# Kernel optimization log

Hardware: AMD Instinct MI355X
Metric: run time of the kernel (lower is better)

The kernel has to match this reference:

```python
import jax, jax.numpy as jnp
import numpy as np

B, N, N0, HH, WW = 4, 3136, 12544, 112, 112
C_IN, C_HID, C_OUT = 128, 512, 128
EPS = 1e-6
BN_EPS = 1e-5


def _grid_idx(loc_orig, H, W):
    # loc_orig [B,N0,2] in [-1,1] -> flat grid index [B,N0]
    loc = jnp.clip(loc_orig, -1.0, 1.0) * 0.5 + 0.5
    gx = jnp.clip(jnp.round(loc[..., 0] * (W - 1)).astype(jnp.int32), 0, W - 1)
    gy = jnp.clip(jnp.round(loc[..., 1] * (H - 1)).astype(jnp.int32), 0, H - 1)
    return gy * W + gx


def token2map(tokens, loc_orig, idx_agg, H, W):
    # tokens [B,N,C] -> dense map [B,C,H,W] (count-averaged scatter)
    Bs, Nt, C = tokens.shape
    Np = loc_orig.shape[1]
    idx_hw = _grid_idx(loc_orig, H, W)                       # [B,N0]
    feat = jnp.take_along_axis(tokens, idx_agg[..., None].astype(jnp.int32), axis=1)  # [B,N0,C]
    seg = (idx_hw + jnp.arange(Bs, dtype=jnp.int32)[:, None] * (H * W)).reshape(-1)
    sums = jax.ops.segment_sum(feat.reshape(Bs * Np, C), seg, num_segments=Bs * H * W)
    cnt = jax.ops.segment_sum(jnp.ones((Bs * Np,), tokens.dtype), seg, num_segments=Bs * H * W)
    out = sums / (cnt[:, None] + EPS)
    return out.reshape(Bs, H, W, C).transpose(0, 3, 1, 2)


def map2token(x_map, Nt, loc_orig, idx_agg, agg_weight, H, W):
    # x_map [B,C,H,W] -> tokens [B,N,C] (agg_weight-normalized gather+scatter)
    Bs, C = x_map.shape[0], x_map.shape[1]
    Np = loc_orig.shape[1]
    idx_hw = _grid_idx(loc_orig, H, W)                       # [B,N0]
    flat = x_map.reshape(Bs, C, H * W).transpose(0, 2, 1)    # [B,HW,C]
    feat = jnp.take_along_axis(flat, idx_hw[..., None], axis=1)  # [B,N0,C]
    seg = (idx_agg.astype(jnp.int32) + jnp.arange(Bs, dtype=jnp.int32)[:, None] * Nt).reshape(-1)
    num = jax.ops.segment_sum((agg_weight[..., None] * feat).reshape(Bs * Np, C), seg, num_segments=Bs * Nt)
    den = jax.ops.segment_sum(agg_weight.reshape(-1), seg, num_segments=Bs * Nt)
    return (num / (den[:, None] + EPS)).reshape(Bs, Nt, C)


def bn(x, g, b):
    # BatchNorm (training-mode batch stats) over x [B,C,N]
    mu = jnp.mean(x, axis=(0, 2), keepdims=True)
    var = jnp.var(x, axis=(0, 2), keepdims=True)
    return (x - mu) * jax.lax.rsqrt(var + BN_EPS) * g[None, :, None] + b[None, :, None]


def setup_inputs():
    key = jax.random.key(0)
    ks = jax.random.split(key, 8)
    x = jax.random.normal(ks[0], (B, N, C_IN), jnp.float32)
    loc_orig = jax.random.uniform(ks[1], (B, N0, 2), jnp.float32) * 2.0 - 1.0
    idx_agg = jax.random.randint(ks[2], (B, N0), 0, N, dtype=jnp.int32)
    agg_weight = jax.random.uniform(ks[3], (B, N0), jnp.float32)
    fc1_w = jax.random.normal(ks[4], (C_HID, C_IN), jnp.float32) * 0.02
    fc1_b = jnp.zeros((C_HID,), jnp.float32)
    g1 = jnp.ones((C_HID,), jnp.float32); b1 = jnp.zeros((C_HID,), jnp.float32)
    dw_w = jax.random.normal(ks[5], (C_HID, 1, 3, 3), jnp.float32) * 0.1
    dw_b = jnp.zeros((C_HID,), jnp.float32)
    dws_w = jax.random.normal(ks[6], (C_HID,), jnp.float32) * 0.1
    g2 = jnp.ones((C_HID,), jnp.float32); b2 = jnp.zeros((C_HID,), jnp.float32)
    fc2_w = jax.random.normal(ks[7], (C_OUT, C_HID), jnp.float32) * 0.02
    fc2_b = jnp.zeros((C_OUT,), jnp.float32)
    g3 = jnp.ones((C_OUT,), jnp.float32); b3 = jnp.zeros((C_OUT,), jnp.float32)
    return dict(x=x, loc_orig=loc_orig, idx_agg=idx_agg, agg_weight=agg_weight,
                fc1_w=fc1_w, fc1_b=fc1_b, g1=g1, b1=b1, dw_w=dw_w, dw_b=dw_b,
                dws_w=dws_w, g2=g2, b2=b2, fc2_w=fc2_w, fc2_b=fc2_b,
                g3=g3, b3=b3, H=HH, W=WW)


def reference(x, loc_orig, idx_agg, agg_weight, fc1_w, fc1_b, g1, b1, dw_w, dw_b,
              dws_w, g2, b2, fc2_w, fc2_b, g3, b3, H, W):
    Bs, Nt, _ = x.shape
    # fc1 (1x1 conv) -> BN -> GELU, channel-major layout [B,C,N]
    h = jnp.einsum('bnc,hc->bhn', x, fc1_w) + fc1_b[None, :, None]
    h = jax.nn.gelu(bn(h, g1, b1), approximate=False)
    # token -> map -> depthwise 3x3 -> map -> token
    x_map = token2map(h.transpose(0, 2, 1), loc_orig, idx_agg, H, W)  # [B,hid,H,W]
    x_map = jax.lax.conv_general_dilated(
        x_map, dw_w, (1, 1), 'SAME', feature_group_count=dw_w.shape[0],
        dimension_numbers=('NCHW', 'OIHW', 'NCHW')) + dw_b[None, :, None, None]
    tok = map2token(x_map, Nt, loc_orig, idx_agg, agg_weight, H, W)   # [B,N,hid]
    # depthwise 1x1 skip (per-channel scale, no bias) + map branch
    h = h * dws_w[None, :, None] + tok.transpose(0, 2, 1)
    h = jax.nn.gelu(bn(h, g2, b2), approximate=False)
    # fc2 -> BN -> GELU (dropout p=0 is identity)
    h = jnp.einsum('bhn,oh->bon', h, fc2_w) + fc2_b[None, :, None]
    h = jax.nn.gelu(bn(h, g3, b3), approximate=False)
    return h.transpose(0, 2, 1)  # [B,N,out]
```

## Files before the change

### kernel.cpp

```cpp
#include <hip/hip_runtime.h>
#include <math.h>

constexpr int kB    = 4;
constexpr int kN    = 3136;
constexpr int kN0   = 12544;
constexpr int kH    = 112, kW = 112;
constexpr int kHW   = kH * kW;
constexpr int kCIN  = 128;
constexpr int kCHID = 512;
constexpr int kCOUT = 128;
constexpr int kROWS = kB * kN;
constexpr int kPTS  = kB * kN0;
constexpr int kBHW  = kB * kHW;
constexpr int kSEG  = kBHW + kROWS;
constexpr int kScanBlks = (kSEG + 255) / 256;
constexpr int kDwBlks   = kB * kHW / 16;
constexpr float kEPS  = 1e-6f;
constexpr float kBEPS = 1e-5f;

typedef __attribute__((ext_vector_type(8))) short short8;
typedef __attribute__((ext_vector_type(4))) float f32x4;

__device__ __forceinline__ float gelu_f(float x) {
    return 0.5f * x * (1.0f + erff(x * 0.70710678118654752440f));
}
__device__ __forceinline__ float bf2f(short s) {
    union { unsigned u; float f; } v; v.u = ((unsigned)(unsigned short)s) << 16; return v.f;
}
__device__ __forceinline__ short f2bf(float f) {
    union { float f; unsigned u; } v; v.f = f;
    const unsigned r = v.u + 0x7fffu + ((v.u >> 16) & 1u);
    return (short)(r >> 16);
}

__device__ __forceinline__ void bn_coef_lds(
    const float* __restrict__ gsum, const float* __restrict__ gsq,
    const float* __restrict__ g, const float* __restrict__ bb,
    float invn, float* ssc, float* ssh)
{
    const int c = threadIdx.x * 2;
#pragma unroll
    for (int u = 0; u < 2; ++u) {
        const float m = gsum[c + u] * invn;
        const float v = fmaxf(gsq[c + u] * invn - m * m, 0.f);
        const float sc = g[c + u] * rsqrtf(v + kBEPS);
        ssc[c + u] = sc;
        ssh[c + u] = bb[c + u] - m * sc;
    }
}

template <int OUT16, int STATS>
__global__ __launch_bounds__(256) void gemm_bf16_k(
    const short* __restrict__ A, const short* __restrict__ W,
    const float* __restrict__ bias, void* __restrict__ Cv,
    float* __restrict__ gsum, float* __restrict__ gsq,
    int M, int N, int K)
{
    __shared__ float ls[64], lq[64];
    if (STATS) {
        if (threadIdx.x < 64) { ls[threadIdx.x] = 0.f; lq[threadIdx.x] = 0.f; }
        __syncthreads();
    }
    const int wave = threadIdx.x >> 6;
    const int lane = threadIdx.x & 63;
    const int r = lane & 15, kg = lane >> 4;
    const int bm = blockIdx.x * 64 + wave * 16;
    const int bn = blockIdx.y * 64;
    const short* arow = A + (size_t)(bm + r) * K + kg * 8;
    f32x4 acc[4];
#pragma unroll
    for (int j = 0; j < 4; ++j) {
        const float bz = bias[bn + j * 16 + r];
        acc[j][0] = bz; acc[j][1] = bz; acc[j][2] = bz; acc[j][3] = bz;
    }
    for (int k0 = 0; k0 < K; k0 += 32) {
        const short8 av = *(const short8*)(arow + k0);
#pragma unroll
        for (int j = 0; j < 4; ++j) {
            const short8 bv = *(const short8*)(W + (size_t)(bn + j * 16 + r) * K + k0 + kg * 8);
            acc[j] = __builtin_amdgcn_mfma_f32_16x16x32_bf16(av, bv, acc[j], 0, 0, 0);
        }
    }
#pragma unroll
    for (int j = 0; j < 4; ++j)
#pragma unroll
        for (int q = 0; q < 4; ++q) {
            const size_t idx = (size_t)(bm + kg * 4 + q) * N + bn + j * 16 + r;
            if constexpr (OUT16) ((short*)Cv)[idx] = f2bf(acc[j][q]);
            else                 ((float*)Cv)[idx] = acc[j][q];
        }
    if (STATS) {
#pragma unroll
        for (int j = 0; j < 4; ++j) {
            const float s = acc[j][0] + acc[j][1] + acc[j][2] + acc[j][3];
            const float q = acc[j][0]*acc[j][0] + acc[j][1]*acc[j][1]
                          + acc[j][2]*acc[j][2] + acc[j][3]*acc[j][3];
            atomicAdd(&ls[j * 16 + r], s);
            atomicAdd(&lq[j * 16 + r], q);
        }
        __syncthreads();
        if (threadIdx.x < 64) {
            atomicAdd(&gsum[bn + threadIdx.x], ls[threadIdx.x]);
            atomicAdd(&gsq[bn + threadIdx.x],  lq[threadIdx.x]);
        }
    }
}

__device__ __forceinline__ void cvt8(const float* __restrict__ in, short* __restrict__ out) {
    const float4 v0 = ((const float4*)in)[0];
    const float4 v1 = ((const float4*)in)[1];
    short8 o;
    o[0] = f2bf(v0.x); o[1] = f2bf(v0.y); o[2] = f2bf(v0.z); o[3] = f2bf(v0.w);
    o[4] = f2bf(v1.x); o[5] = f2bf(v1.y); o[6] = f2bf(v1.z); o[7] = f2bf(v1.w);
    *(short8*)out = o;
}

constexpr int kCVT8    = (kROWS * kCIN + 512 * 128 + 128 * 512) / 8;
constexpr int kCvtBlks = (kCVT8 + 9 * 512 + 255) / 256;
constexpr int kCntBlks = kPTS / 256;

__global__ void prep_k(const float* __restrict__ x, short* __restrict__ xb,
                       const float* __restrict__ w1, short* __restrict__ w1b,
                       const float* __restrict__ w2, short* __restrict__ w2b,
                       const float* __restrict__ dww, short* __restrict__ wTb,
                       const float* __restrict__ loc, const int* __restrict__ iagg,
                       int* __restrict__ ihw, int* __restrict__ cnt)
{
    const int blk = blockIdx.x;
    if (blk < kCvtBlks) {
        const int i = blk * 256 + threadIdx.x;
        constexpr int na = kROWS * kCIN, nb = 512 * 128;
        if (i < kCVT8) {
            int t = i * 8;
            if (t < na) { cvt8(x + t, xb + t); return; }
            t -= na;
            if (t < nb) { cvt8(w1 + t, w1b + t); return; }
            t -= nb;
            cvt8(w2 + t, w2b + t);
            return;
        }
        const int j = i - kCVT8;
        if (j < 9 * 512) {
            const int tap = j / 512, ch = j % 512;
            wTb[j] = f2bf(dww[ch * 9 + tap]);
        }
        return;
    }
    const int p = (blk - kCvtBlks) * 256 + threadIdx.x;
    if (p >= kPTS) return;
    float lx = loc[(size_t)p * 2 + 0];
    float ly = loc[(size_t)p * 2 + 1];
    lx = fminf(fmaxf(lx, -1.f), 1.f) * 0.5f + 0.5f;
    ly = fminf(fmaxf(ly, -1.f), 1.f) * 0.5f + 0.5f;
    int gx = (int)rintf(lx * (float)(kW - 1)); gx = min(max(gx, 0), kW - 1);
    int gy = (int)rintf(ly * (float)(kH - 1)); gy = min(max(gy, 0), kH - 1);
    const int idx = gy * kW + gx;
    ihw[p] = idx;
    const int b = p / kN0;
    atomicAdd(cnt + b * kHW + idx, 1);
    atomicAdd(cnt + kBHW + b * kN + iagg[p], 1);
}

__global__ __launch_bounds__(256) void scan1_k(const int* __restrict__ cnt,
                                               int* __restrict__ off, int* __restrict__ bsum)
{
    __shared__ int sh[256];
    const int t = threadIdx.x;
    const int i = blockIdx.x * 256 + t;
    const int v = (i < kSEG) ? cnt[i] : 0;
    sh[t] = v; __syncthreads();
#pragma unroll
    for (int o = 1; o < 256; o <<= 1) {
        const int tmp = (t >= o) ? sh[t - o] : 0;
        __syncthreads();
        sh[t] += tmp;
        __syncthreads();
    }
    if (i < kSEG) off[i] = sh[t] - v;
    if (t == 255) bsum[blockIdx.x] = sh[255];
}

__global__ __launch_bounds__(256) void scan23_k(int* __restrict__ off,
                                                const int* __restrict__ bsum)
{
    __shared__ int sh[256];
    const int t = threadIdx.x;
    const int v = (t < kScanBlks) ? bsum[t] : 0;
    sh[t] = v; __syncthreads();
#pragma unroll
    for (int o = 1; o < 256; o <<= 1) {
        const int tmp = (t >= o) ? sh[t - o] : 0;
        __syncthreads();
        sh[t] += tmp;
        __syncthreads();
    }
    const int add = sh[blockIdx.x] - bsum[blockIdx.x];
    const int i = blockIdx.x * 256 + t;
    if (i < kSEG) off[i] += add;
}

__global__ void fill_k(const int* __restrict__ iagg, const int* __restrict__ ihw,
                       const float* __restrict__ aw, int* __restrict__ off,
                       int* __restrict__ slotA, float* __restrict__ w_all)
{
    const int p = blockIdx.x * 256 + threadIdx.x;
    if (p >= kPTS) return;
    const int b = p / kN0;
    const int tokrow = b * kN + iagg[p];
    const int cell   = b * kHW + ihw[p];
    const int cpos = atomicAdd(off + cell, 1);
    slotA[cpos] = tokrow;
    const int tpos = atomicAdd(off + kBHW + tokrow, 1);
    slotA[tpos] = cell;
    w_all[tpos] = aw[p];
}

__global__ __launch_bounds__(256) void colstats_b(
    const short* __restrict__ X, float* __restrict__ gsum, float* __restrict__ gsq,
    int rows_per_blk)
{
    __shared__ float shs[4][512];
    __shared__ float shq[4][512];
    const int g = threadIdx.x & 63;
    const int rr = threadIdx.x >> 6;
    const int r0 = blockIdx.x * rows_per_blk;
    float s[8] = {}, q[8] = {};
    for (int r = rr; r < rows_per_blk; r += 4) {
        const short8 v = *(const short8*)(X + (size_t)(r0 + r) * kCHID + g * 8);
#pragma unroll
        for (int j = 0; j < 8; ++j) { const float f = bf2f(v[j]); s[j] += f; q[j] += f * f; }
    }
#pragma unroll
    for (int j = 0; j < 8; ++j) { shs[rr][g * 8 + j] = s[j]; shq[rr][g * 8 + j] = q[j]; }
    __syncthreads();
    const int c = threadIdx.x * 2;
    const float s0 = shs[0][c] + shs[1][c] + shs[2][c] + shs[3][c];
    const float s1 = shs[0][c+1] + shs[1][c+1] + shs[2][c+1] + shs[3][c+1];
    const float q0 = shq[0][c] + shq[1][c] + shq[2][c] + shq[3][c];
    const float q1 = shq[0][c+1] + shq[1][c+1] + shq[2][c+1] + shq[3][c+1];
    atomicAdd(&gsum[c], s0);   atomicAdd(&gsum[c+1], s1);
    atomicAdd(&gsq[c],  q0);   atomicAdd(&gsq[c+1],  q1);
}

__global__ __launch_bounds__(256) void bn_act_b(
    const short* __restrict__ in, short* __restrict__ out,
    const float* __restrict__ gsum, const float* __restrict__ gsq,
    const float* __restrict__ g, const float* __restrict__ bb, float invn)
{
    __shared__ float ssc[512], ssh[512];
    bn_coef_lds(gsum, gsq, g, bb, invn, ssc, ssh);
    __syncthreads();
    const size_t i = (size_t)blockIdx.x * 256 + threadIdx.x;
    const int c0 = (int)(i & 63) * 8;
    const short8 v = *(const short8*)(in + i * 8);
    short8 o;
#pragma unroll
    for (int j = 0; j < 8; ++j)
        o[j] = f2bf(gelu_f(fmaf(bf2f(v[j]), ssc[c0 + j], ssh[c0 + j])));
    *(short8*)(out + i * 8) = o;
}

__global__ __launch_bounds__(256) void bn_act_f128(
    const float* __restrict__ in, float* __restrict__ out,
    const float* __restrict__ gsum, const float* __restrict__ gsq,
    const float* __restrict__ g, const float* __restrict__ bb, float invn)
{
    __shared__ float ssc[128], ssh[128];
    if (threadIdx.x < 128) {
        const int c = threadIdx.x;
        const float m = gsum[c] * invn;
        const float v = fmaxf(gsq[c] * invn - m * m, 0.f);
        const float sc = g[c] * rsqrtf(v + kBEPS);
        ssc[c] = sc;
        ssh[c] = bb[c] - m * sc;
    }
    __syncthreads();
    const size_t i = (size_t)blockIdx.x * 256 + threadIdx.x;
    const int c0 = (int)(i & 31) * 4;
    float4 v = ((const float4*)in)[i];
    v.x = gelu_f(fmaf(v.x, ssc[c0 + 0], ssh[c0 + 0]));
    v.y = gelu_f(fmaf(v.y, ssc[c0 + 1], ssh[c0 + 1]));
    v.z = gelu_f(fmaf(v.z, ssc[c0 + 2], ssh[c0 + 2]));
    v.w = gelu_f(fmaf(v.w, ssc[c0 + 3], ssh[c0 + 3]));
    ((float4*)out)[i] = v;
}

__global__ __launch_bounds__(256) void gather_map_b(
    const short* __restrict__ hb, const int* __restrict__ off,
    const int* __restrict__ toklist, short* __restrict__ smap)
{
    const int lane = threadIdx.x & 63;
    const int cell = blockIdx.x * 4 + (threadIdx.x >> 6);
    const int s = cell ? off[cell - 1] : 0;
    const int e = off[cell];
    const int c0 = lane * 8;
    float a[8] = {};
    int j = s;
    for (; j + 1 < e; j += 2) {
        const int t0 = toklist[j], t1 = toklist[j + 1];
        const short8 v0 = *(const short8*)(hb + (size_t)t0 * kCHID + c0);
        const short8 v1 = *(const short8*)(hb + (size_t)t1 * kCHID + c0);
#pragma unroll
        for (int t = 0; t < 8; ++t) a[t] += bf2f(v0[t]) + bf2f(v1[t]);
    }
    if (j < e) {
        const short8 v = *(const short8*)(hb + (size_t)toklist[j] * kCHID + c0);
#pragma unroll
        for (int t = 0; t < 8; ++t) a[t] += bf2f(v[t]);
    }
    const float sc = 1.f / ((float)(e - s) + kEPS);
    short8 o;
#pragma unroll
    for (int t = 0; t < 8; ++t) o[t] = f2bf(a[t] * sc);
    *(short8*)(smap + (size_t)cell * kCHID + c0) = o;
}

__global__ __launch_bounds__(256) void dwconv_b(
    const short* __restrict__ smap, const int* __restrict__ cnt,
    const short* __restrict__ wTb, const float* __restrict__ bdw,
    short* __restrict__ convo)
{
    constexpr int kTX = kW / 2;
    constexpr int kChunk = kDwBlks / 8;
    const int wg = (blockIdx.x & 7) * kChunk + (blockIdx.x >> 3);
    const int c8 = threadIdx.x & 63;
    const int w  = wg * 4 + (threadIdx.x >> 6);
    const int b   = w / (kTX * kTX);
    const int rem = w % (kTX * kTX);
    const int ty = rem / kTX, tx = rem % kTX;
    const int y0 = ty * 2, x0 = tx * 2;
    const int gbase = b * kHW;
    const int c0 = c8 * 8;

    const int cell00 = gbase + y0 * kW + x0;
    const int2 nA = *(const int2*)(cnt + cell00);
    const int2 nB = *(const int2*)(cnt + cell00 + kW);
    const int n00 = nA.x, n01 = nA.y, n10 = nB.x, n11 = nB.y;
    if ((n00 | n01 | n10 | n11) == 0) return;

    float wf[9][8];
#pragma unroll
    for (int t = 0; t < 9; ++t) {
        const short8 wv = *(const short8*)(wTb + t * kCHID + c0);
#pragma unroll
        for (int j = 0; j < 8; ++j) wf[t][j] = bf2f(wv[j]);
    }
    float bz[8];
    {
        const float4 b0 = *(const float4*)(bdw + c0);
        const float4 b1 = *(const float4*)(bdw + c0 + 4);
        bz[0] = b0.x; bz[1] = b0.y; bz[2] = b0.z; bz[3] = b0.w;
        bz[4] = b1.x; bz[5] = b1.y; bz[6] = b1.z; bz[7] = b1.w;
    }
    float acc[2][2][8];
#pragma unroll
    for (int cy = 0; cy < 2; ++cy)
#pragma unroll
        for (int cx = 0; cx < 2; ++cx)
#pragma unroll
            for (int j = 0; j < 8; ++j) acc[cy][cx][j] = bz[j];

#pragma unroll
    for (int dy = 0; dy < 4; ++dy) {
        const int yy = y0 - 1 + dy;
        if ((unsigned)yy >= (unsigned)kH) continue;
#pragma unroll
        for (int dx = 0; dx < 4; ++dx) {
            const int xx = x0 - 1 + dx;
            if ((unsigned)xx >= (unsigned)kW) continue;
            const short8 tv = *(const short8*)(smap + (size_t)(gbase + yy * kW + xx) * kCHID + c0);
            float tf[8];
#pragma unroll
            for (int j = 0; j < 8; ++j) tf[j] = bf2f(tv[j]);
#pragma unroll
            for (int cy = 0; cy < 2; ++cy) {
                const int wy = dy - cy;
                if ((unsigned)wy >= 3u) continue;
#pragma unroll
                for (int cx = 0; cx < 2; ++cx) {
                    const int wx = dx - cx;
                    if ((unsigned)wx >= 3u) continue;
                    const float* wq = wf[wy * 3 + wx];
#pragma unroll
                    for (int j = 0; j < 8; ++j)
                        acc[cy][cx][j] = fmaf(wq[j], tf[j], acc[cy][cx][j]);
                }
            }
        }
    }
#pragma unroll
    for (int cy = 0; cy < 2; ++cy)
#pragma unroll
        for (int cx = 0; cx < 2; ++cx) {
            const int n = (cy == 0) ? (cx == 0 ? n00 : n01) : (cx == 0 ? n10 : n11);
            if (!n) continue;
            short8 o;
#pragma unroll
            for (int j = 0; j < 8; ++j) o[j] = f2bf(acc[cy][cx][j]);
            *(short8*)(convo + (size_t)(cell00 + cy * kW + cx) * kCHID + c0) = o;
        }
}

__global__ __launch_bounds__(256) void gather_tok_b(
    const short* __restrict__ convo, const int* __restrict__ off,
    const int* __restrict__ celllist, const float* __restrict__ wlist,
    const short* __restrict__ hb, const float* __restrict__ dws,
    short* __restrict__ h2)
{
    const int lane = threadIdx.x & 63;
    const int wave = threadIdx.x >> 6;
    const int t = blockIdx.x * 4 + wave;
    const int seg = kBHW + t;
    const int sbeg = off[seg - 1], send = off[seg];
    const int c0 = lane * 8;
    const float4 d0 = *(const float4*)(dws + c0);
    const float4 d1 = *(const float4*)(dws + c0 + 4);
    const float dd[8] = {d0.x, d0.y, d0.z, d0.w, d1.x, d1.y, d1.z, d1.w};
    float a[8] = {};
    float den = 0.f;
    int j = sbeg;
    for (; j + 1 < send; j += 2) {
        const float w0 = wlist[j], w1 = wlist[j + 1];
        const int   cA = celllist[j], cB = celllist[j + 1];
        den += w0 + w1;
        const short8 v0 = *(const short8*)(convo + (size_t)cA * kCHID + c0);
        const short8 v1 = *(const short8*)(convo + (size_t)cB * kCHID + c0);
#pragma unroll
        for (int k = 0; k < 8; ++k)
            a[k] += w0 * bf2f(v0[k]) + w1 * bf2f(v1[k]);
    }
    if (j < send) {
        const float w = wlist[j];
        den += w;
        const short8 v = *(const short8*)(convo + (size_t)celllist[j] * kCHID + c0);
#pragma unroll
        for (int k = 0; k < 8; ++k) a[k] = fmaf(w, bf2f(v[k]), a[k]);
    }
    const float r = 1.f / (den + kEPS);
    const short8 hv = *(const short8*)(hb + (size_t)t * kCHID + c0);
    short8 o;
#pragma unroll
    for (int k = 0; k < 8; ++k)
        o[k] = f2bf(fmaf(bf2f(hv[k]), dd[k], a[k] * r));
    *(short8*)(h2 + (size_t)t * kCHID + c0) = o;
}

extern "C" void kernel_launch(void* const* d_in, const int* in_sizes, int n_in,
                              void* d_out, int out_size, void* d_ws, size_t ws_size,
                              hipStream_t stream)
{
    (void)in_sizes; (void)n_in; (void)out_size; (void)ws_size;
    const float* x    = (const float*)d_in[0];
    const float* loc  = (const float*)d_in[1];
    const int*   iagg = (const int*)  d_in[2];
    const float* aw   = (const float*)d_in[3];
    const float* fc1w = (const float*)d_in[4];
    const float* fc1b = (const float*)d_in[5];
    const float* g1   = (const float*)d_in[6];
    const float* b1   = (const float*)d_in[7];
    const float* dww  = (const float*)d_in[8];
    const float* dwb  = (const float*)d_in[9];
    const float* dwsw = (const float*)d_in[10];
    const float* g2   = (const float*)d_in[11];
    const float* b2   = (const float*)d_in[12];
    const float* fc2w = (const float*)d_in[13];
    const float* fc2b = (const float*)d_in[14];
    const float* g3   = (const float*)d_in[15];
    const float* b3   = (const float*)d_in[16];
    float* outp = (float*)d_out;

    float* ws = (float*)d_ws;
    float* gsum1 = ws + 0;
    float* gsq1  = ws + 512;
    float* gsum2 = ws + 1024;
    float* gsq2  = ws + 1536;
    float* gsum3 = ws + 2048;
    float* gsq3  = ws + 2176;
    int* cnt = (int*)(ws + 2304);
    const size_t zero_bytes = (2304ull + kSEG) * 4;
    int*   off   = cnt + kSEG;
    int*   bsum  = off + 62724;
    int*   ihw   = bsum + 256;
    int*   slotA = ihw + kPTS;
    float* w_all = (float*)(slotA + 2 * kPTS);
    short* wTb   = (short*)(w_all + 2 * kPTS);
    short* xb    = wTb + 4608;
    short* w1b   = xb + (size_t)kROWS * kCIN;
    short* w2b   = w1b + 512 * 128;
    short* hraw  = w2b + 128 * 512;
    short* hb16  = hraw + (size_t)kROWS * kCHID;
    short* smap  = hb16 + (size_t)kROWS * kCHID;
    short* convo = smap + (size_t)kBHW * kCHID;
    float* out3  = (float*)smap;

    hipMemsetAsync(ws, 0, zero_bytes, stream);

    prep_k<<<kCvtBlks + kCntBlks, 256, 0, stream>>>(
        x, xb, fc1w, w1b, fc2w, w2b, dww, wTb, loc, iagg, ihw, cnt);

    gemm_bf16_k<1, 1><<<dim3(kROWS / 64, kCHID / 64), 256, 0, stream>>>(
        xb, w1b, fc1b, hraw, gsum1, gsq1, kROWS, kCHID, kCIN);

    scan1_k<<<kScanBlks, 256, 0, stream>>>(cnt, off, bsum);
    scan23_k<<<kScanBlks, 256, 0, stream>>>(off, bsum);
    fill_k<<<kPTS / 256, 256, 0, stream>>>(iagg, ihw, aw, off, slotA, w_all);

    bn_act_b<<<(kROWS * kCHID / 8) / 256, 256, 0, stream>>>(
        hraw, hb16, gsum1, gsq1, g1, b1, 1.f / kROWS);

    gather_map_b<<<kBHW / 4, 256, 0, stream>>>(hb16, off, slotA, smap);
    dwconv_b<<<kDwBlks, 256, 0, stream>>>(smap, cnt, wTb, dwb, convo);

    gather_tok_b<<<kROWS / 4, 256, 0, stream>>>(convo, off, slotA, w_all,
                                                hb16, dwsw, hraw);

    colstats_b<<<196, 256, 0, stream>>>(hraw, gsum2, gsq2, 64);
    bn_act_b<<<(kROWS * kCHID / 8) / 256, 256, 0, stream>>>(
        hraw, hb16, gsum2, gsq2, g2, b2, 1.f / kROWS);

    gemm_bf16_k<0, 1><<<dim3(kROWS / 64, kCOUT / 64), 256, 0, stream>>>(
        hb16, w2b, fc2b, out3, gsum3, gsq3, kROWS, kCOUT, kCHID);

    bn_act_f128<<<(kROWS * kCOUT / 4) / 256, 256, 0, stream>>>(
        out3, outp, gsum3, gsq3, g3, b3, 1.f / kROWS);
}
```

Measured before the change: 193.2 us.

## Fuse token-to-map gather into depthwise conv via shared-memory halo tiles

Merges the gather_map and dwconv kernels into one kernel. Each block builds a 10x10 halo tile for a 128-channel quarter in LDS by gathering the tokens of each cell, then runs the 3x3 depthwise conv on the 8x8 interior. This removes the full smap write and read in global memory and one launch. In exchange, halo cells are gathered redundantly (about 1.56x), and blocks whose cells are all empty still do the gather work, because the old early exit on empty 2x2 groups is gone.

```diff
diff --git a/kernel.cpp b/kernel.cpp
--- a/kernel.cpp
+++ b/kernel.cpp
@@ -14,7 +14,7 @@
 constexpr int kBHW  = kB * kHW;
 constexpr int kSEG  = kBHW + kROWS;
 constexpr int kScanBlks = (kSEG + 255) / 256;
-constexpr int kDwBlks   = kB * kHW / 16;
+constexpr int kTileBlks = 4 * 196 * 4;
 constexpr float kEPS  = 1e-6f;
 constexpr float kBEPS = 1e-5f;
 
@@ -285,120 +285,98 @@
     ((float4*)out)[i] = v;
 }
 
-__global__ __launch_bounds__(256) void gather_map_b(
+__global__ __launch_bounds__(256) void gmap_conv_k(
     const short* __restrict__ hb, const int* __restrict__ off,
-    const int* __restrict__ toklist, short* __restrict__ smap)
-{
-    const int lane = threadIdx.x & 63;
-    const int cell = blockIdx.x * 4 + (threadIdx.x >> 6);
-    const int s = cell ? off[cell - 1] : 0;
-    const int e = off[cell];
-    const int c0 = lane * 8;
-    float a[8] = {};
-    int j = s;
-    for (; j + 1 < e; j += 2) {
-        const int t0 = toklist[j], t1 = toklist[j + 1];
-        const short8 v0 = *(const short8*)(hb + (size_t)t0 * kCHID + c0);
-        const short8 v1 = *(const short8*)(hb + (size_t)t1 * kCHID + c0);
-#pragma unroll
-        for (int t = 0; t < 8; ++t) a[t] += bf2f(v0[t]) + bf2f(v1[t]);
-    }
-    if (j < e) {
-        const short8 v = *(const short8*)(hb + (size_t)toklist[j] * kCHID + c0);
-#pragma unroll
-        for (int t = 0; t < 8; ++t) a[t] += bf2f(v[t]);
-    }
-    const float sc = 1.f / ((float)(e - s) + kEPS);
-    short8 o;
-#pragma unroll
-    for (int t = 0; t < 8; ++t) o[t] = f2bf(a[t] * sc);
-    *(short8*)(smap + (size_t)cell * kCHID + c0) = o;
-}
-
-__global__ __launch_bounds__(256) void dwconv_b(
-    const short* __restrict__ smap, const int* __restrict__ cnt,
+    const int* __restrict__ toklist, const int* __restrict__ cnt,
     const short* __restrict__ wTb, const float* __restrict__ bdw,
     short* __restrict__ convo)
 {
-    constexpr int kTX = kW / 2;
-    constexpr int kChunk = kDwBlks / 8;
+    __shared__ short tile[10 * 10 * 128];
+    constexpr int kChunk = kTileBlks / 8;
     const int wg = (blockIdx.x & 7) * kChunk + (blockIdx.x >> 3);
-    const int c8 = threadIdx.x & 63;
-    const int w  = wg * 4 + (threadIdx.x >> 6);
-    const int b   = w / (kTX * kTX);
-    const int rem = w % (kTX * kTX);
-    const int ty = rem / kTX, tx = rem % kTX;
-    const int y0 = ty * 2, x0 = tx * 2;
+    const int q  = wg & 3;
+    const int t  = wg >> 2;
+    const int b   = t / 196;
+    const int rem = t % 196;
+    const int ty = rem / 14, tx = rem % 14;
+    const int y0 = ty * 8, x0 = tx * 8;
     const int gbase = b * kHW;
-    const int c0 = c8 * 8;
-
-    const int cell00 = gbase + y0 * kW + x0;
-    const int2 nA = *(const int2*)(cnt + cell00);
-    const int2 nB = *(const int2*)(cnt + cell00 + kW);
-    const int n00 = nA.x, n01 = nA.y, n10 = nB.x, n11 = nB.y;
-    if ((n00 | n01 | n10 | n11) == 0) return;
+    const int cg = threadIdx.x & 15;
+    const int co = q * 128 + cg * 8;
+    const int csub = threadIdx.x >> 4;
+
+    for (int i = 0; i < 7; ++i) {
+        const int cell = i * 16 + csub;
+        if (cell < 100) {
+            const int cy = cell / 10, cx = cell % 10;
+            const int y = y0 - 1 + cy, x = x0 - 1 + cx;
+            float a[8] = {};
+            float scn = 0.f;
+            if ((unsigned)y < (unsigned)kH && (unsigned)x < (unsigned)kW) {
+                const int gcell = gbase + y * kW + x;
+                const int s = gcell ? off[gcell - 1] : 0;
+                const int e = off[gcell];
+                int j = s;
+                for (; j + 1 < e; j += 2) {
+                    const int t0 = toklist[j], t1 = toklist[j + 1];
+                    const short8 v0 = *(const short8*)(hb + (size_t)t0 * kCHID + co);
+                    const short8 v1 = *(const short8*)(hb + (size_t)t1 * kCHID + co);
+#pragma unroll
+                    for (int k = 0; k < 8; ++k) a[k] += bf2f(v0[k]) + bf2f(v1[k]);
+                }
+                if (j < e) {
+                    const short8 v = *(const short8*)(hb + (size_t)toklist[j] * kCHID + co);
+#pragma unroll
+                    for (int k = 0; k < 8; ++k) a[k] += bf2f(v[k]);
+                }
+                scn = 1.f / ((float)(e - s) + kEPS);
+            }
+            short8 o;
+#pragma unroll
+            for (int k = 0; k < 8; ++k) o[k] = f2bf(a[k] * scn);
+            *(short8*)(tile + cell * 128 + cg * 8) = o;
+        }
+    }
+    __syncthreads();
 
     float wf[9][8];
 #pragma unroll
-    for (int t = 0; t < 9; ++t) {
-        const short8 wv = *(const short8*)(wTb + t * kCHID + c0);
-#pragma unroll
-        for (int j = 0; j < 8; ++j) wf[t][j] = bf2f(wv[j]);
+    for (int tap = 0; tap < 9; ++tap) {
+        const short8 wv = *(const short8*)(wTb + tap * kCHID + co);
+#pragma unroll
+        for (int j = 0; j < 8; ++j) wf[tap][j] = bf2f(wv[j]);
     }
     float bz[8];
     {
-        const float4 b0 = *(const float4*)(bdw + c0);
-        const float4 b1 = *(const float4*)(bdw + c0 + 4);
+        const float4 b0 = *(const float4*)(bdw + co);
+        const float4 b1 = *(const float4*)(bdw + co + 4);
         bz[0] = b0.x; bz[1] = b0.y; bz[2] = b0.z; bz[3] = b0.w;
         bz[4] = b1.x; bz[5] = b1.y; bz[6] = b1.z; bz[7] = b1.w;
     }
-    float acc[2][2][8];
-#pragma unroll
-    for (int cy = 0; cy < 2; ++cy)
-#pragma unroll
-        for (int cx = 0; cx < 2; ++cx)
-#pragma unroll
-            for (int j = 0; j < 8; ++j) acc[cy][cx][j] = bz[j];
-
-#pragma unroll
-    for (int dy = 0; dy < 4; ++dy) {
-        const int yy = y0 - 1 + dy;
-        if ((unsigned)yy >= (unsigned)kH) continue;
-#pragma unroll
-        for (int dx = 0; dx < 4; ++dx) {
-            const int xx = x0 - 1 + dx;
-            if ((unsigned)xx >= (unsigned)kW) continue;
-            const short8 tv = *(const short8*)(smap + (size_t)(gbase + yy * kW + xx) * kCHID + c0);
-            float tf[8];
-#pragma unroll
-            for (int j = 0; j < 8; ++j) tf[j] = bf2f(tv[j]);
-#pragma unroll
-            for (int cy = 0; cy < 2; ++cy) {
-                const int wy = dy - cy;
-                if ((unsigned)wy >= 3u) continue;
-#pragma unroll
-                for (int cx = 0; cx < 2; ++cx) {
-                    const int wx = dx - cx;
-                    if ((unsigned)wx >= 3u) continue;
-                    const float* wq = wf[wy * 3 + wx];
-#pragma unroll
-                    for (int j = 0; j < 8; ++j)
-                        acc[cy][cx][j] = fmaf(wq[j], tf[j], acc[cy][cx][j]);
-                }
+#pragma unroll
+    for (int i = 0; i < 4; ++i) {
+        const int cell = csub + 16 * i;
+        const int oy = cell >> 3, ox = cell & 7;
+        const int gcell = gbase + (y0 + oy) * kW + (x0 + ox);
+        if (cnt[gcell] == 0) continue;
+        float acc[8];
+#pragma unroll
+        for (int j = 0; j < 8; ++j) acc[j] = bz[j];
+#pragma unroll
+        for (int dy = 0; dy < 3; ++dy)
+#pragma unroll
+            for (int dx = 0; dx < 3; ++dx) {
+                const short8 tv = *(const short8*)(tile + ((oy + dy) * 10 + ox + dx) * 128 + cg * 8);
+                const float* wq = wf[dy * 3 + dx];
+#pragma unroll
+                for (int j = 0; j < 8; ++j)
+                    acc[j] = fmaf(wq[j], bf2f(tv[j]), acc[j]);
             }
-        }
-    }
-#pragma unroll
-    for (int cy = 0; cy < 2; ++cy)
-#pragma unroll
-        for (int cx = 0; cx < 2; ++cx) {
-            const int n = (cy == 0) ? (cx == 0 ? n00 : n01) : (cx == 0 ? n10 : n11);
-            if (!n) continue;
-            short8 o;
-#pragma unroll
-            for (int j = 0; j < 8; ++j) o[j] = f2bf(acc[cy][cx][j]);
-            *(short8*)(convo + (size_t)(cell00 + cy * kW + cx) * kCHID + c0) = o;
-        }
+        short8 o;
+#pragma unroll
+        for (int j = 0; j < 8; ++j) o[j] = f2bf(acc[j]);
+        *(short8*)(convo + (size_t)gcell * kCHID + co) = o;
+    }
 }
 
 __global__ __launch_bounds__(256) void gather_tok_b(
@@ -489,9 +467,8 @@
     short* w2b   = w1b + 512 * 128;
     short* hraw  = w2b + 128 * 512;
     short* hb16  = hraw + (size_t)kROWS * kCHID;
-    short* smap  = hb16 + (size_t)kROWS * kCHID;
-    short* convo = smap + (size_t)kBHW * kCHID;
-    float* out3  = (float*)smap;
+    short* convo = hb16 + (size_t)kROWS * kCHID;
+    float* out3  = (float*)convo;
 
     hipMemsetAsync(ws, 0, zero_bytes, stream);
 
@@ -508,8 +485,7 @@
     bn_act_b<<<(kROWS * kCHID / 8) / 256, 256, 0, stream>>>(
         hraw, hb16, gsum1, gsq1, g1, b1, 1.f / kROWS);
 
-    gather_map_b<<<kBHW / 4, 256, 0, stream>>>(hb16, off, slotA, smap);
-    dwconv_b<<<kDwBlks, 256, 0, stream>>>(smap, cnt, wTb, dwb, convo);
+    gmap_conv_k<<<kTileBlks, 256, 0, stream>>>(hb16, off, slotA, cnt, wTb, dwb, convo);
 
     gather_tok_b<<<kROWS / 4, 256, 0, stream>>>(convo, off, slotA, w_all,
                                                 hb16, dwsw, hraw);
```

Measured after the change: 209.5 us. 8.5% more time.

## Fuse input cast and BN2+GELU into GEMM A-operand loads

Applied to the files above, without the earlier changes.

The fc1 GEMM now reads fp32 x directly and converts it to bf16 while loading, so the separate cast of x in the prep kernel goes away. The fc2 GEMM applies BN2 scale/shift and GELU to raw bf16 activations as it loads them, using per-block LDS coefficients, which removes a standalone elementwise kernel and its full-tensor write and read. In exchange, erf-based GELU is recomputed once per column block in the fc2 GEMM, and every block redundantly computes the BN coefficients.

```diff
diff --git a/kernel.cpp b/kernel.cpp
--- a/kernel.cpp
+++ b/kernel.cpp
@@ -49,24 +49,30 @@
     }
 }
 
-template <int OUT16, int STATS>
+template <int AMODE, int OUT16, int STATS>
 __global__ __launch_bounds__(256) void gemm_bf16_k(
-    const short* __restrict__ A, const short* __restrict__ W,
+    const void* __restrict__ Av, const short* __restrict__ W,
     const float* __restrict__ bias, void* __restrict__ Cv,
     float* __restrict__ gsum, float* __restrict__ gsq,
+    const float* __restrict__ gsumA, const float* __restrict__ gsqA,
+    const float* __restrict__ gA, const float* __restrict__ bA,
     int M, int N, int K)
 {
     __shared__ float ls[64], lq[64];
+    __shared__ float ssc[512], ssh[512];
+    if (AMODE == 2)
+        bn_coef_lds(gsumA, gsqA, gA, bA, 1.f / kROWS, ssc, ssh);
     if (STATS) {
         if (threadIdx.x < 64) { ls[threadIdx.x] = 0.f; lq[threadIdx.x] = 0.f; }
-        __syncthreads();
-    }
+    }
+    if (AMODE == 2 || STATS) __syncthreads();
+
     const int wave = threadIdx.x >> 6;
     const int lane = threadIdx.x & 63;
     const int r = lane & 15, kg = lane >> 4;
     const int bm = blockIdx.x * 64 + wave * 16;
     const int bn = blockIdx.y * 64;
-    const short* arow = A + (size_t)(bm + r) * K + kg * 8;
+    const size_t arow_off = (size_t)(bm + r) * K + kg * 8;
     f32x4 acc[4];
 #pragma unroll
     for (int j = 0; j < 4; ++j) {
@@ -74,7 +80,22 @@
         acc[j][0] = bz; acc[j][1] = bz; acc[j][2] = bz; acc[j][3] = bz;
     }
     for (int k0 = 0; k0 < K; k0 += 32) {
-        const short8 av = *(const short8*)(arow + k0);
+        short8 av;
+        if constexpr (AMODE == 0) {
+            av = *(const short8*)((const short*)Av + arow_off + k0);
+        } else if constexpr (AMODE == 1) {
+            const float* af = (const float*)Av + arow_off + k0;
+            const float4 f0 = ((const float4*)af)[0];
+            const float4 f1 = ((const float4*)af)[1];
+            av[0] = f2bf(f0.x); av[1] = f2bf(f0.y); av[2] = f2bf(f0.z); av[3] = f2bf(f0.w);
+            av[4] = f2bf(f1.x); av[5] = f2bf(f1.y); av[6] = f2bf(f1.z); av[7] = f2bf(f1.w);
+        } else {
+            const short8 raw = *(const short8*)((const short*)Av + arow_off + k0);
+            const int cb = k0 + kg * 8;
+#pragma unroll
+            for (int j = 0; j < 8; ++j)
+                av[j] = f2bf(gelu_f(fmaf(bf2f(raw[j]), ssc[cb + j], ssh[cb + j])));
+        }
 #pragma unroll
         for (int j = 0; j < 4; ++j) {
             const short8 bv = *(const short8*)(W + (size_t)(bn + j * 16 + r) * K + k0 + kg * 8);
@@ -115,12 +136,11 @@
     *(short8*)out = o;
 }
 
-constexpr int kCVT8    = (kROWS * kCIN + 512 * 128 + 128 * 512) / 8;
+constexpr int kCVT8    = (512 * 128 + 128 * 512) / 8;
 constexpr int kCvtBlks = (kCVT8 + 9 * 512 + 255) / 256;
 constexpr int kCntBlks = kPTS / 256;
 
-__global__ void prep_k(const float* __restrict__ x, short* __restrict__ xb,
-                       const float* __restrict__ w1, short* __restrict__ w1b,
+__global__ void prep_k(const float* __restrict__ w1, short* __restrict__ w1b,
                        const float* __restrict__ w2, short* __restrict__ w2b,
                        const float* __restrict__ dww, short* __restrict__ wTb,
                        const float* __restrict__ loc, const int* __restrict__ iagg,
@@ -129,11 +149,9 @@
     const int blk = blockIdx.x;
     if (blk < kCvtBlks) {
         const int i = blk * 256 + threadIdx.x;
-        constexpr int na = kROWS * kCIN, nb = 512 * 128;
+        constexpr int nb = 512 * 128;
         if (i < kCVT8) {
             int t = i * 8;
-            if (t < na) { cvt8(x + t, xb + t); return; }
-            t -= na;
             if (t < nb) { cvt8(w1 + t, w1b + t); return; }
             t -= nb;
             cvt8(w2 + t, w2b + t);
@@ -413,6 +431,7 @@
     const int seg = kBHW + t;
     const int sbeg = off[seg - 1], send = off[seg];
     const int c0 = lane * 8;
+    const short8 hv = *(const short8*)(hb + (size_t)t * kCHID + c0);
     const float4 d0 = *(const float4*)(dws + c0);
     const float4 d1 = *(const float4*)(dws + c0 + 4);
     const float dd[8] = {d0.x, d0.y, d0.z, d0.w, d1.x, d1.y, d1.z, d1.w};
@@ -421,10 +440,10 @@
     int j = sbeg;
     for (; j + 1 < send; j += 2) {
         const float w0 = wlist[j], w1 = wlist[j + 1];
-        const int   cA = celllist[j], cB = celllist[j + 1];
+        const int   cA = celllist[j], cBn = celllist[j + 1];
         den += w0 + w1;
-        const short8 v0 = *(const short8*)(convo + (size_t)cA * kCHID + c0);
-        const short8 v1 = *(const short8*)(convo + (size_t)cB * kCHID + c0);
+        const short8 v0 = *(const short8*)(convo + (size_t)cA  * kCHID + c0);
+        const short8 v1 = *(const short8*)(convo + (size_t)cBn * kCHID + c0);
 #pragma unroll
         for (int k = 0; k < 8; ++k)
             a[k] += w0 * bf2f(v0[k]) + w1 * bf2f(v1[k]);
@@ -437,7 +456,6 @@
         for (int k = 0; k < 8; ++k) a[k] = fmaf(w, bf2f(v[k]), a[k]);
     }
     const float r = 1.f / (den + kEPS);
-    const short8 hv = *(const short8*)(hb + (size_t)t * kCHID + c0);
     short8 o;
 #pragma unroll
     for (int k = 0; k < 8; ++k)
@@ -484,8 +502,7 @@
     int*   slotA = ihw + kPTS;
     float* w_all = (float*)(slotA + 2 * kPTS);
     short* wTb   = (short*)(w_all + 2 * kPTS);
-    short* xb    = wTb + 4608;
-    short* w1b   = xb + (size_t)kROWS * kCIN;
+    short* w1b   = wTb + 4608;
     short* w2b   = w1b + 512 * 128;
     short* hraw  = w2b + 128 * 512;
     short* hb16  = hraw + (size_t)kROWS * kCHID;
@@ -496,10 +513,11 @@
     hipMemsetAsync(ws, 0, zero_bytes, stream);
 
     prep_k<<<kCvtBlks + kCntBlks, 256, 0, stream>>>(
-        x, xb, fc1w, w1b, fc2w, w2b, dww, wTb, loc, iagg, ihw, cnt);
-
-    gemm_bf16_k<1, 1><<<dim3(kROWS / 64, kCHID / 64), 256, 0, stream>>>(
-        xb, w1b, fc1b, hraw, gsum1, gsq1, kROWS, kCHID, kCIN);
+        fc1w, w1b, fc2w, w2b, dww, wTb, loc, iagg, ihw, cnt);
+
+    gemm_bf16_k<1, 1, 1><<<dim3(kROWS / 64, kCHID / 64), 256, 0, stream>>>(
+        x, w1b, fc1b, hraw, gsum1, gsq1,
+        nullptr, nullptr, nullptr, nullptr, kROWS, kCHID, kCIN);
 
     scan1_k<<<kScanBlks, 256, 0, stream>>>(cnt, off, bsum);
     scan23_k<<<kScanBlks, 256, 0, stream>>>(off, bsum);
@@ -515,11 +533,10 @@
                                                 hb16, dwsw, hraw);
 
     colstats_b<<<196, 256, 0, stream>>>(hraw, gsum2, gsq2, 64);
-    bn_act_b<<<(kROWS * kCHID / 8) / 256, 256, 0, stream>>>(
-        hraw, hb16, gsum2, gsq2, g2, b2, 1.f / kROWS);
-
-    gemm_bf16_k<0, 1><<<dim3(kROWS / 64, kCOUT / 64), 256, 0, stream>>>(
-        hb16, w2b, fc2b, out3, gsum3, gsq3, kROWS, kCOUT, kCHID);
+
+    gemm_bf16_k<2, 0, 1><<<dim3(kROWS / 64, kCOUT / 64), 256, 0, stream>>>(
+        hraw, w2b, fc2b, out3, gsum3, gsq3,
+        gsum2, gsq2, g2, b2, kROWS, kCOUT, kCHID);
 
     bn_act_f128<<<(kROWS * kCOUT / 4) / 256, 256, 0, stream>>>(
         out3, outp, gsum3, gsq3, g3, b3, 1.f / kROWS);
```

Result: slower. 199.2 us (+3.1%).

## Store GEMM operands in k-block-major layout for coalesced MFMA loads

Applied to the files above, without the earlier changes.

The GEMM operands (x, fc1/fc2 weights, and the second BN-GELU output) are now written in a [K/8][rows][8] k-block-major layout. Each MFMA fragment load of 8 bf16 values then reads consecutive rows contiguously instead of striding by K. Prep and the second bn_act kernel do the transposition while writing, which trades coalesced writes there for coalesced reads in the GEMMs. The load of hv in gather_tok is hoisted ahead of the accumulation loop.

```diff
diff --git a/kernel.cpp b/kernel.cpp
--- a/kernel.cpp
+++ b/kernel.cpp
@@ -50,7 +50,7 @@
 }
 
 template <int OUT16, int STATS>
-__global__ __launch_bounds__(256) void gemm_bf16_k(
+__global__ __launch_bounds__(256) void gemm_kb_k(
     const short* __restrict__ A, const short* __restrict__ W,
     const float* __restrict__ bias, void* __restrict__ Cv,
     float* __restrict__ gsum, float* __restrict__ gsq,
@@ -66,7 +66,6 @@
     const int r = lane & 15, kg = lane >> 4;
     const int bm = blockIdx.x * 64 + wave * 16;
     const int bn = blockIdx.y * 64;
-    const short* arow = A + (size_t)(bm + r) * K + kg * 8;
     f32x4 acc[4];
 #pragma unroll
     for (int j = 0; j < 4; ++j) {
@@ -74,10 +73,11 @@
         acc[j][0] = bz; acc[j][1] = bz; acc[j][2] = bz; acc[j][3] = bz;
     }
     for (int k0 = 0; k0 < K; k0 += 32) {
-        const short8 av = *(const short8*)(arow + k0);
+        const int kb = (k0 >> 3) + kg;
+        const short8 av = *(const short8*)(A + ((size_t)kb * M + bm + r) * 8);
 #pragma unroll
         for (int j = 0; j < 4; ++j) {
-            const short8 bv = *(const short8*)(W + (size_t)(bn + j * 16 + r) * K + k0 + kg * 8);
+            const short8 bv = *(const short8*)(W + ((size_t)kb * N + bn + j * 16 + r) * 8);
             acc[j] = __builtin_amdgcn_mfma_f32_16x16x32_bf16(av, bv, acc[j], 0, 0, 0);
         }
     }
@@ -106,7 +106,13 @@
     }
 }
 
-__device__ __forceinline__ void cvt8(const float* __restrict__ in, short* __restrict__ out) {
+constexpr int kXBlks  = kROWS * (kCIN / 8) / 256;
+constexpr int kW1Blks = kCHID * (kCIN / 8) / 256;
+constexpr int kW2Blks = kCOUT * (kCHID / 8) / 256;
+constexpr int kWtBlks = (9 * 512 + 255) / 256;
+constexpr int kCntBlks = kPTS / 256;
+
+__device__ __forceinline__ void cvt8_to(const float* __restrict__ in, short* __restrict__ out) {
     const float4 v0 = ((const float4*)in)[0];
     const float4 v1 = ((const float4*)in)[1];
     short8 o;
@@ -115,38 +121,45 @@
     *(short8*)out = o;
 }
 
-constexpr int kCVT8    = (kROWS * kCIN + 512 * 128 + 128 * 512) / 8;
-constexpr int kCvtBlks = (kCVT8 + 9 * 512 + 255) / 256;
-constexpr int kCntBlks = kPTS / 256;
-
-__global__ void prep_k(const float* __restrict__ x, short* __restrict__ xb,
-                       const float* __restrict__ w1, short* __restrict__ w1b,
-                       const float* __restrict__ w2, short* __restrict__ w2b,
+__global__ void prep_k(const float* __restrict__ x, short* __restrict__ xt,
+                       const float* __restrict__ w1, short* __restrict__ w1t,
+                       const float* __restrict__ w2, short* __restrict__ w2t,
                        const float* __restrict__ dww, short* __restrict__ wTb,
                        const float* __restrict__ loc, const int* __restrict__ iagg,
                        int* __restrict__ ihw, int* __restrict__ cnt)
 {
-    const int blk = blockIdx.x;
-    if (blk < kCvtBlks) {
+    int blk = blockIdx.x;
+    if (blk < kXBlks) {
         const int i = blk * 256 + threadIdx.x;
-        constexpr int na = kROWS * kCIN, nb = 512 * 128;
-        if (i < kCVT8) {
-            int t = i * 8;
-            if (t < na) { cvt8(x + t, xb + t); return; }
-            t -= na;
-            if (t < nb) { cvt8(w1 + t, w1b + t); return; }
-            t -= nb;
-            cvt8(w2 + t, w2b + t);
-            return;
-        }
-        const int j = i - kCVT8;
+        const int m = i >> 4, kb = i & 15;
+        cvt8_to(x + (size_t)m * kCIN + kb * 8, xt + ((size_t)kb * kROWS + m) * 8);
+        return;
+    }
+    blk -= kXBlks;
+    if (blk < kW1Blks) {
+        const int i = blk * 256 + threadIdx.x;
+        const int n = i >> 4, kb = i & 15;
+        cvt8_to(w1 + (size_t)n * kCIN + kb * 8, w1t + ((size_t)kb * kCHID + n) * 8);
+        return;
+    }
+    blk -= kW1Blks;
+    if (blk < kW2Blks) {
+        const int i = blk * 256 + threadIdx.x;
+        const int n = i >> 6, kb = i & 63;
+        cvt8_to(w2 + (size_t)n * kCHID + kb * 8, w2t + ((size_t)kb * kCOUT + n) * 8);
+        return;
+    }
+    blk -= kW2Blks;
+    if (blk < kWtBlks) {
+        const int j = blk * 256 + threadIdx.x;
         if (j < 9 * 512) {
             const int tap = j / 512, ch = j % 512;
             wTb[j] = f2bf(dww[ch * 9 + tap]);
         }
         return;
     }
-    const int p = (blk - kCvtBlks) * 256 + threadIdx.x;
+    blk -= kWtBlks;
+    const int p = blk * 256 + threadIdx.x;
     if (p >= kPTS) return;
     float lx = loc[(size_t)p * 2 + 0];
     float ly = loc[(size_t)p * 2 + 1];
@@ -242,6 +255,7 @@
     atomicAdd(&gsq[c],  q0);   atomicAdd(&gsq[c+1],  q1);
 }
 
+template <int KB>
 __global__ __launch_bounds__(256) void bn_act_b(
     const short* __restrict__ in, short* __restrict__ out,
     const float* __restrict__ gsum, const float* __restrict__ gsq,
@@ -251,13 +265,16 @@
     bn_coef_lds(gsum, gsq, g, bb, invn, ssc, ssh);
     __syncthreads();
     const size_t i = (size_t)blockIdx.x * 256 + threadIdx.x;
-    const int c0 = (int)(i & 63) * 8;
+    const int cg = (int)(i & 63);
+    const int c0 = cg * 8;
+    const size_t row = i >> 6;
     const short8 v = *(const short8*)(in + i * 8);
     short8 o;
 #pragma unroll
     for (int j = 0; j < 8; ++j)
         o[j] = f2bf(gelu_f(fmaf(bf2f(v[j]), ssc[c0 + j], ssh[c0 + j])));
-    *(short8*)(out + i * 8) = o;
+    if constexpr (KB) *(short8*)(out + ((size_t)cg * kROWS + row) * 8) = o;
+    else              *(short8*)(out + i * 8) = o;
 }
 
 __global__ __launch_bounds__(256) void bn_act_f128(
@@ -413,6 +430,7 @@
     const int seg = kBHW + t;
     const int sbeg = off[seg - 1], send = off[seg];
     const int c0 = lane * 8;
+    const short8 hv = *(const short8*)(hb + (size_t)t * kCHID + c0);
     const float4 d0 = *(const float4*)(dws + c0);
     const float4 d1 = *(const float4*)(dws + c0 + 4);
     const float dd[8] = {d0.x, d0.y, d0.z, d0.w, d1.x, d1.y, d1.z, d1.w};
@@ -421,10 +439,10 @@
     int j = sbeg;
     for (; j + 1 < send; j += 2) {
         const float w0 = wlist[j], w1 = wlist[j + 1];
-        const int   cA = celllist[j], cB = celllist[j + 1];
+        const int   cA = celllist[j], cBn = celllist[j + 1];
         den += w0 + w1;
-        const short8 v0 = *(const short8*)(convo + (size_t)cA * kCHID + c0);
-        const short8 v1 = *(const short8*)(convo + (size_t)cB * kCHID + c0);
+        const short8 v0 = *(const short8*)(convo + (size_t)cA  * kCHID + c0);
+        const short8 v1 = *(const short8*)(convo + (size_t)cBn * kCHID + c0);
 #pragma unroll
         for (int k = 0; k < 8; ++k)
             a[k] += w0 * bf2f(v0[k]) + w1 * bf2f(v1[k]);
@@ -437,7 +455,6 @@
         for (int k = 0; k < 8; ++k) a[k] = fmaf(w, bf2f(v[k]), a[k]);
     }
     const float r = 1.f / (den + kEPS);
-    const short8 hv = *(const short8*)(hb + (size_t)t * kCHID + c0);
     short8 o;
 #pragma unroll
     for (int k = 0; k < 8; ++k)
@@ -484,10 +501,10 @@
     int*   slotA = ihw + kPTS;
     float* w_all = (float*)(slotA + 2 * kPTS);
     short* wTb   = (short*)(w_all + 2 * kPTS);
-    short* xb    = wTb + 4608;
-    short* w1b   = xb + (size_t)kROWS * kCIN;
-    short* w2b   = w1b + 512 * 128;
-    short* hraw  = w2b + 128 * 512;
+    short* xt    = wTb + 4608;
+    short* w1t   = xt + (size_t)kROWS * kCIN;
+    short* w2t   = w1t + 512 * 128;
+    short* hraw  = w2t + 128 * 512;
     short* hb16  = hraw + (size_t)kROWS * kCHID;
     short* smap  = hb16 + (size_t)kROWS * kCHID;
     short* convo = smap + (size_t)kBHW * kCHID;
@@ -495,17 +512,17 @@
 
     hipMemsetAsync(ws, 0, zero_bytes, stream);
 
-    prep_k<<<kCvtBlks + kCntBlks, 256, 0, stream>>>(
-        x, xb, fc1w, w1b, fc2w, w2b, dww, wTb, loc, iagg, ihw, cnt);
-
-    gemm_bf16_k<1, 1><<<dim3(kROWS / 64, kCHID / 64), 256, 0, stream>>>(
-        xb, w1b, fc1b, hraw, gsum1, gsq1, kROWS, kCHID, kCIN);
+    prep_k<<<kXBlks + kW1Blks + kW2Blks + kWtBlks + kCntBlks, 256, 0, stream>>>(
+        x, xt, fc1w, w1t, fc2w, w2t, dww, wTb, loc, iagg, ihw, cnt);
+
+    gemm_kb_k<1, 1><<<dim3(kROWS / 64, kCHID / 64), 256, 0, stream>>>(
+        xt, w1t, fc1b, hraw, gsum1, gsq1, kROWS, kCHID, kCIN);
 
     scan1_k<<<kScanBlks, 256, 0, stream>>>(cnt, off, bsum);
     scan23_k<<<kScanBlks, 256, 0, stream>>>(off, bsum);
     fill_k<<<kPTS / 256, 256, 0, stream>>>(iagg, ihw, aw, off, slotA, w_all);
 
-    bn_act_b<<<(kROWS * kCHID / 8) / 256, 256, 0, stream>>>(
+    bn_act_b<0><<<(kROWS * kCHID / 8) / 256, 256, 0, stream>>>(
         hraw, hb16, gsum1, gsq1, g1, b1, 1.f / kROWS);
 
     gather_map_b<<<kBHW / 4, 256, 0, stream>>>(hb16, off, slotA, smap);
@@ -515,11 +532,11 @@
                                                 hb16, dwsw, hraw);
 
     colstats_b<<<196, 256, 0, stream>>>(hraw, gsum2, gsq2, 64);
-    bn_act_b<<<(kROWS * kCHID / 8) / 256, 256, 0, stream>>>(
+    bn_act_b<1><<<(kROWS * kCHID / 8) / 256, 256, 0, stream>>>(
         hraw, hb16, gsum2, gsq2, g2, b2, 1.f / kROWS);
 
-    gemm_bf16_k<0, 1><<<dim3(kROWS / 64, kCOUT / 64), 256, 0, stream>>>(
-        hb16, w2b, fc2b, out3, gsum3, gsq3, kROWS, kCOUT, kCHID);
+    gemm_kb_k<0, 1><<<dim3(kROWS / 64, kCOUT / 64), 256, 0, stream>>>(
+        hb16, w2t, fc2b, out3, gsum3, gsq3, kROWS, kCOUT, kCHID);
 
     bn_act_f128<<<(kROWS * kCOUT / 4) / 256, 256, 0, stream>>>(
         out3, outp, gsum3, gsq3, g3, b3, 1.f / kROWS);
```

After: 173.2 us. 10.3% less time.
